# Optimization experiments

Measured on AMD Instinct MI355X. Metric: run time of the kernel, lower is better.

Reference implementation:

```python
import jax, jax.numpy as jnp
import numpy as np

# Grid / problem constants (match init_kwargs: shape=[15,400,400], batch_size=2)
B, D, H, W = 2, 15, 400, 400
N = 200000          # active voxels
CIN, COUT = 32, 64
# 27 kernel offsets for ksize=3, dilation=1, centered (submanifold alignment)
OFFS = np.array([[dz, dy, dx]
                 for dz in (-1, 0, 1)
                 for dy in (-1, 0, 1)
                 for dx in (-1, 0, 1)], dtype=np.int32)  # [27, 3]


def setup_inputs() -> dict:
    rng = np.random.default_rng(0)
    # unique active voxel coordinates (sorted flat indices for locality)
    flat = np.sort(rng.choice(B * D * H * W, size=N, replace=False)).astype(np.int64)
    b = flat // (D * H * W)
    r = flat % (D * H * W)
    z = r // (H * W)
    r = r % (H * W)
    y = r // W
    x = r % W
    coors = jnp.asarray(np.stack([b, z, y, x], axis=1).astype(np.int32))  # [N,4]

    key = jax.random.key(0)
    k1, k2, k3 = jax.random.split(key, 3)
    features = jax.random.normal(k1, (N, CIN), jnp.float32)
    W1 = jax.random.normal(k2, (27, CIN, COUT), jnp.float32) * (1.0 / np.sqrt(27.0 * CIN))
    W2 = jax.random.normal(k3, (27, COUT, COUT), jnp.float32) * (1.0 / np.sqrt(27.0 * COUT))
    return {"features": features, "coors": coors, "batch_size": B, "W1": W1, "W2": W2}


def _neighbor_table(coors):
    """Rulebook: for each of 27 offsets, index of the neighboring active voxel (-1 if none)."""
    n = coors.shape[0]
    flat = ((coors[:, 0] * D + coors[:, 1]) * H + coors[:, 2]) * W + coors[:, 3]
    # dense voxel hash: flat coord -> row index, -1 = inactive
    table = jnp.full((B * D * H * W,), -1, jnp.int32).at[flat].set(
        jnp.arange(n, dtype=jnp.int32))
    offs = jnp.asarray(OFFS)  # [27,3]
    z = coors[None, :, 1] + offs[:, 0:1]  # [27,N]
    y = coors[None, :, 2] + offs[:, 1:2]
    x = coors[None, :, 3] + offs[:, 2:3]
    valid = (z >= 0) & (z < D) & (y >= 0) & (y < H) & (x >= 0) & (x < W)
    nflat = ((coors[None, :, 0] * D + jnp.clip(z, 0, D - 1)) * H
             + jnp.clip(y, 0, H - 1)) * W + jnp.clip(x, 0, W - 1)
    nbr = table[nflat]                      # [27, N]
    return jnp.where(valid, nbr, -1)


def _subm_conv(feats, nbr, Wk):
    """Gather-GEMM-scatter submanifold conv: out[i] = sum_k W[k] @ feats[nbr[k,i]]."""
    out = jnp.zeros((feats.shape[0], Wk.shape[-1]), feats.dtype)
    for k in range(nbr.shape[0]):  # fixed 27-iteration loop over kernel offsets
        j = nbr[k]
        valid = j >= 0
        g = jnp.where(valid[:, None], feats[jnp.where(valid, j, 0)], 0.0)  # [N,Cin]
        out = out + g @ Wk[k]
    return out


def reference(features, coors, batch_size, W1, W2):
    # Submanifold conv preserves the active set -> rulebook is shared by both layers.
    nbr = _neighbor_table(coors)
    x = _subm_conv(features, nbr, W1)   # [N, COUT]
    x = _subm_conv(x, nbr, W2)          # [N, COUT]
    return x
```

## Files before the change

kernel.cpp:

```cpp
#include <hip/hip_runtime.h>
#include <hip/hip_bf16.h>

#define DD 15
#define HH 400
#define WW 400
#define CIN 32
#define COUT 64
#define KK 27
#define NVOX (2 * DD * HH * WW)
#define NWORDS (NVOX / 64)
#define CAP 32768
#define CNT_STRIDE 64
#define OFFC_GRID 2048
#define PCAP 262144
#define SCAN_B 1024

typedef short bf16x8 __attribute__((ext_vector_type(8)));
typedef float f32x4  __attribute__((ext_vector_type(4)));

__device__ inline short f2bf(float f) {
    unsigned u = __float_as_uint(f);
    return (short)((u + 0x7FFFu + ((u >> 16) & 1u)) >> 16);
}
__device__ inline float bflo(unsigned u) { return __uint_as_float(u << 16); }
__device__ inline float bfhi(unsigned u) { return __uint_as_float(u & 0xFFFF0000u); }

__global__ void init_kernel(unsigned long long* __restrict__ bitmap,
                            int* __restrict__ cnt) {
    int t = blockIdx.x * blockDim.x + threadIdx.x;
    if (t < KK * CNT_STRIDE) cnt[t] = 0;
    int stride = gridDim.x * blockDim.x;
    for (int w = t; w < NWORDS; w += stride) bitmap[w] = 0ull;
}

__global__ void fill_kernel(const int* __restrict__ coors,
                            int* __restrict__ flats,
                            unsigned long long* __restrict__ bitmap, int n) {
    int i = blockIdx.x * blockDim.x + threadIdx.x;
    if (i >= n) return;
    int b = coors[i * 4 + 0];
    int z = coors[i * 4 + 1];
    int y = coors[i * 4 + 2];
    int x = coors[i * 4 + 3];
    int f = ((b * DD + z) * HH + y) * WW + x;
    flats[i] = f;
    atomicOr(&bitmap[f >> 6], 1ull << (f & 63));
}

__global__ void prefix_kernel(const int* __restrict__ flats,
                              int* __restrict__ prefix, int n) {
    int w = blockIdx.x * blockDim.x + threadIdx.x;
    if (w >= NWORDS) return;
    int target = w << 6;
    int lo = 0, hi = n;
    while (lo < hi) {
        int mid = (lo + hi) >> 1;
        if (flats[mid] < target) lo = mid + 1; else hi = mid;
    }
    prefix[w] = lo;
}

__device__ inline bool bm_test(const unsigned long long* __restrict__ bitmap, int f) {
    return (bitmap[f >> 6] >> (f & 63)) & 1ull;
}
__device__ inline int bm_rank(const unsigned long long* __restrict__ bitmap,
                              const int* __restrict__ prefix, int f) {
    int w = f >> 6, b = f & 63;
    unsigned long long m = bitmap[w];
    return prefix[w] + __popcll(m & ((1ull << b) - 1ull));
}

__global__ __launch_bounds__(256) void build_pairs_kernel(
        const int* __restrict__ flats,
        const unsigned long long* __restrict__ bitmap,
        const int* __restrict__ prefix,
        int* __restrict__ cnt, int* __restrict__ pairI,
        int* __restrict__ pairJ, int* __restrict__ percnt, int n) {
    __shared__ int lcnt[KK];
    __shared__ int lbase[KK];
    __shared__ int lpos[KK];
    int i = blockIdx.x * blockDim.x + threadIdx.x;
    if (threadIdx.x < KK) { lcnt[threadIdx.x] = 0; lpos[threadIdx.x] = 0; }
    __syncthreads();

    int f0 = 0, x = 0;
    unsigned vmask = 0;
    bool act = (i < n);
    if (act) {
        f0 = flats[i];
        x = f0 % WW;
        int rem = f0 / WW;
        int y = rem % HH;
        int z = (rem / HH) % DD;
#pragma unroll
        for (int p = 0; p < 9; ++p) {
            int dz = p / 3 - 1, dy = p % 3 - 1;
            int zn = z + dz, yn = y + dy;
            if (zn < 0 || zn >= DD || yn < 0 || yn >= HH) continue;
            int fn = f0 + dz * (HH * WW) + dy * WW;
            int kb = p * 3;
            if (x > 0 && bm_test(bitmap, fn - 1)) {
                vmask |= 1u << kb; atomicAdd(&lcnt[kb], 1);
            }
            if (kb + 1 != 13 && bm_test(bitmap, fn)) {
                vmask |= 1u << (kb + 1); atomicAdd(&lcnt[kb + 1], 1);
            }
            if (x < WW - 1 && bm_test(bitmap, fn + 1)) {
                vmask |= 1u << (kb + 2); atomicAdd(&lcnt[kb + 2], 1);
            }
        }
        percnt[i] = __popc(vmask);
    }
    __syncthreads();
    if (threadIdx.x < KK && lcnt[threadIdx.x] > 0)
        lbase[threadIdx.x] = atomicAdd(&cnt[threadIdx.x * CNT_STRIDE], lcnt[threadIdx.x]);
    __syncthreads();
    if (act && vmask) {
        int lt = 0;
#pragma unroll
        for (int p = 0; p < 9; ++p) {
            int kb = p * 3;
            if (!(vmask & (7u << kb))) continue;
            int dz = p / 3 - 1, dy = p % 3 - 1;
            int fn = f0 + dz * (HH * WW) + dy * WW;
#pragma unroll
            for (int d = 0; d < 3; ++d) {
                int k = kb + d;
                if (!(vmask & (1u << k))) continue;
                int j = bm_rank(bitmap, prefix, fn + d - 1);
                int pos = lbase[k] + atomicAdd(&lpos[k], 1);
                if (pos < CAP) {
                    pairI[k * CAP + pos] = (i << 5) | lt;
                    pairJ[k * CAP + pos] = j;
                }
                ++lt;
            }
        }
    }
}

__global__ void pad_pairs_kernel(const int* __restrict__ cnt,
                                 int* __restrict__ pairI,
                                 int* __restrict__ pairJ, int n) {
    int k = blockIdx.x;
    int ck = min(cnt[k * CNT_STRIDE], CAP);
    int ckp = min((ck + 127) & ~127, CAP);
    for (int pos = ck + (int)threadIdx.x; pos < ckp; pos += blockDim.x) {
        pairI[k * CAP + pos] = (n << 5);
        pairJ[k * CAP + pos] = 0;
    }
}

__global__ void scan1_kernel(const int* __restrict__ pc, int* __restrict__ bsum, int n) {
    __shared__ int red[256];
    int base = blockIdx.x * SCAN_B;
    int s = 0;
#pragma unroll
    for (int u = 0; u < 4; ++u) {
        int idx = base + u * 256 + threadIdx.x;
        if (idx < n) s += pc[idx];
    }
    red[threadIdx.x] = s; __syncthreads();
    for (int o = 128; o > 0; o >>= 1) {
        if ((int)threadIdx.x < o) red[threadIdx.x] += red[threadIdx.x + o];
        __syncthreads();
    }
    if (threadIdx.x == 0) bsum[blockIdx.x] = red[0];
}

__global__ void scan2_kernel(int* __restrict__ bsum, int nb) {
    __shared__ int s[256];
    int v = ((int)threadIdx.x < nb) ? bsum[threadIdx.x] : 0;
    s[threadIdx.x] = v; __syncthreads();
    for (int o = 1; o < 256; o <<= 1) {
        int t = ((int)threadIdx.x >= o) ? s[threadIdx.x - o] : 0;
        __syncthreads();
        s[threadIdx.x] += t;
        __syncthreads();
    }
    if ((int)threadIdx.x < nb) bsum[threadIdx.x] = s[threadIdx.x] - v;
}

__global__ void scan3_kernel(const int* __restrict__ pc, const int* __restrict__ bsum,
                             int* __restrict__ rowptr, int n) {
    __shared__ int ts[256];
    int base = blockIdx.x * SCAN_B + threadIdx.x * 4;
    int e[4]; int s = 0;
#pragma unroll
    for (int u = 0; u < 4; ++u) {
        int idx = base + u;
        e[u] = (idx < n) ? pc[idx] : 0;
        s += e[u];
    }
    ts[threadIdx.x] = s; __syncthreads();
    for (int o = 1; o < 256; o <<= 1) {
        int t = ((int)threadIdx.x >= o) ? ts[threadIdx.x - o] : 0;
        __syncthreads();
        ts[threadIdx.x] += t;
        __syncthreads();
    }
    int run = ts[threadIdx.x] - s + bsum[blockIdx.x];
#pragma unroll
    for (int u = 0; u < 4; ++u) {
        int idx = base + u;
        if (idx < n) rowptr[idx] = run;
        run += e[u];
        if (idx == n - 1) rowptr[n] = run;
    }
}

template <int C>
__global__ __launch_bounds__(256) void center_mfma_kernel(
        const float* __restrict__ xin, const float* __restrict__ Wc,
        const int* __restrict__ rowptr, const unsigned short* __restrict__ part,
        float* __restrict__ xout, int n) {
    constexpr int KT = C / 32;
    int lane = threadIdx.x & 63;
    int mrow = lane & 15;
    int kgrp = lane >> 4;
    int wid = (blockIdx.x * blockDim.x + threadIdx.x) >> 6;
    int nwaves = (gridDim.x * blockDim.x) >> 6;

    bf16x8 bf[KT][4];
#pragma unroll
    for (int kt = 0; kt < KT; ++kt)
#pragma unroll
        for (int nt = 0; nt < 4; ++nt)
#pragma unroll
            for (int j = 0; j < 8; ++j)
                bf[kt][nt][j] = f2bf(Wc[(kt * 32 + kgrp * 8 + j) * 64 + nt * 16 + mrow]);

    int ntiles = (n + 15) >> 4;
    for (int t = wid; t < ntiles; t += nwaves) {
        int row = t * 16 + mrow;
        f32x4 zero = {0.f, 0.f, 0.f, 0.f};
        bf16x8 a[KT];
        if (row < n) {
            const float* xr = xin + (size_t)row * C + kgrp * 8;
#pragma unroll
            for (int kt = 0; kt < KT; ++kt) {
                float4 x0 = *(const float4*)(xr + kt * 32);
                float4 x1 = *(const float4*)(xr + kt * 32 + 4);
                a[kt][0] = f2bf(x0.x); a[kt][1] = f2bf(x0.y);
                a[kt][2] = f2bf(x0.z); a[kt][3] = f2bf(x0.w);
                a[kt][4] = f2bf(x1.x); a[kt][5] = f2bf(x1.y);
                a[kt][6] = f2bf(x1.z); a[kt][7] = f2bf(x1.w);
            }
        } else {
#pragma unroll
            for (int kt = 0; kt < KT; ++kt)
#pragma unroll
                for (int j = 0; j < 8; ++j) a[kt][j] = 0;
        }
        f32x4 acc[4];
#pragma unroll
        for (int nt = 0; nt < 4; ++nt) {
            acc[nt] = zero;
#pragma unroll
            for (int kt = 0; kt < KT; ++kt)
                acc[nt] = __builtin_amdgcn_mfma_f32_16x16x32_bf16(a[kt], bf[kt][nt], acc[nt], 0, 0, 0);
        }
#pragma unroll
        for (int r = 0; r < 4; ++r) {
            int orow = t * 16 + kgrp * 4 + r;
            if (orow < n) {
                int s0 = rowptr[orow], s1 = rowptr[orow + 1];
                for (int s = s0; s < s1; ++s) {
                    uint2 q = *(const uint2*)(part + (size_t)s * 64 + mrow * 4);
                    acc[0][r] += bflo(q.x);
                    acc[1][r] += bfhi(q.x);
                    acc[2][r] += bflo(q.y);
                    acc[3][r] += bfhi(q.y);
                }
#pragma unroll
                for (int nt = 0; nt < 4; ++nt)
                    xout[(size_t)orow * 64 + nt * 16 + mrow] = acc[nt][r];
            }
        }
    }
}

template <int C>
__global__ __launch_bounds__(256) void offc_mfma_kernel(
        const float* __restrict__ xin, const float* __restrict__ Wsrc,
        const int* __restrict__ cnt, const int* __restrict__ pairI,
        const int* __restrict__ pairJ, const int* __restrict__ rowptr,
        unsigned short* __restrict__ part, int n) {
    constexpr int KT = C / 32;
    __shared__ int pfx[KK + 1];
    int lane = threadIdx.x & 63;
    int wid = threadIdx.x >> 6;
    int mrow = lane & 15;
    int kgrp = lane >> 4;
    if (threadIdx.x == 0) {
        int acc = 0; pfx[0] = 0;
        for (int k = 0; k < KK; ++k) {
            int ck = min(cnt[k * CNT_STRIDE], CAP);
            acc += (ck + 127) >> 7;
            pfx[k + 1] = acc;
        }
    }
    __syncthreads();
    int T = pfx[KK];
    for (int g = blockIdx.x; g < T; g += gridDim.x) {
        int k = 0;
        while (pfx[k + 1] <= g) ++k;
        int chunk = g - pfx[k];
        const float* Wk = Wsrc + (size_t)k * C * 64;
        bf16x8 bf[KT][4];
#pragma unroll
        for (int kt = 0; kt < KT; ++kt)
#pragma unroll
            for (int nt = 0; nt < 4; ++nt)
#pragma unroll
                for (int j = 0; j < 8; ++j)
                    bf[kt][nt][j] = f2bf(Wk[(kt * 32 + kgrp * 8 + j) * 64 + nt * 16 + mrow]);
        int base = k * CAP + chunk * 128 + wid * 32;
#pragma unroll
        for (int half = 0; half < 2; ++half) {
            int b16 = base + half * 16;
            int jrow = pairJ[b16 + mrow];
            const float* xr = xin + (size_t)jrow * C + kgrp * 8;
            bf16x8 a[KT];
#pragma unroll
            for (int kt = 0; kt < KT; ++kt) {
                float4 x0 = *(const float4*)(xr + kt * 32);
                float4 x1 = *(const float4*)(xr + kt * 32 + 4);
                a[kt][0] = f2bf(x0.x); a[kt][1] = f2bf(x0.y);
                a[kt][2] = f2bf(x0.z); a[kt][3] = f2bf(x0.w);
                a[kt][4] = f2bf(x1.x); a[kt][5] = f2bf(x1.y);
                a[kt][6] = f2bf(x1.z); a[kt][7] = f2bf(x1.w);
            }
            f32x4 zero = {0.f, 0.f, 0.f, 0.f};
            f32x4 acc[4];
#pragma unroll
            for (int nt = 0; nt < 4; ++nt) {
                acc[nt] = zero;
#pragma unroll
                for (int kt = 0; kt < KT; ++kt)
                    acc[nt] = __builtin_amdgcn_mfma_f32_16x16x32_bf16(a[kt], bf[kt][nt], acc[nt], 0, 0, 0);
            }
#pragma unroll
            for (int r = 0; r < 4; ++r) {
                int pk = pairI[b16 + kgrp * 4 + r];
                int ir = pk >> 5;
                if (ir < n) {
                    int dst = rowptr[ir] + (pk & 31);
                    if (dst < PCAP) {
                        uint2 q;
                        q.x = (unsigned)(unsigned short)f2bf(acc[0][r]) |
                              ((unsigned)(unsigned short)f2bf(acc[1][r]) << 16);
                        q.y = (unsigned)(unsigned short)f2bf(acc[2][r]) |
                              ((unsigned)(unsigned short)f2bf(acc[3][r]) << 16);
                        *(uint2*)(part + (size_t)dst * 64 + mrow * 4) = q;
                    }
                }
            }
        }
    }
}

extern "C" void kernel_launch(void* const* d_in, const int* in_sizes, int n_in,
                              void* d_out, int out_size, void* d_ws, size_t ws_size,
                              hipStream_t stream) {
    const float* feats = (const float*)d_in[0];
    const int*   coors = (const int*)d_in[1];
    const float* W1 = (const float*)d_in[3];
    const float* W2 = (const float*)d_in[4];
    float* out = (float*)d_out;

    int n = in_sizes[0] / CIN;

    char* ws = (char*)d_ws;
    size_t off = 0;
    float* x1 = (float*)(ws + off);
    off += ((size_t)n * COUT * 4 + 255) & ~(size_t)255;
    unsigned long long* bitmap = (unsigned long long*)(ws + off);
    off += ((size_t)NWORDS * 8 + 255) & ~(size_t)255;
    int* prefix = (int*)(ws + off);
    off += ((size_t)NWORDS * 4 + 255) & ~(size_t)255;
    int* flats = (int*)(ws + off);
    off += ((size_t)n * 4 + 255) & ~(size_t)255;
    int* percnt = (int*)(ws + off);
    off += ((size_t)n * 4 + 255) & ~(size_t)255;
    int* rowptr = (int*)(ws + off);
    off += ((size_t)(n + 1) * 4 + 255) & ~(size_t)255;
    int* bsum = (int*)(ws + off);
    off += (256 * 4 + 255) & ~(size_t)255;
    int* cnt = (int*)(ws + off);
    off += ((size_t)KK * CNT_STRIDE * 4 + 255) & ~(size_t)255;
    int* pairI = (int*)(ws + off);
    off += ((size_t)KK * CAP * 4 + 4096 + 255) & ~(size_t)255;
    int* pairJ = (int*)(ws + off);
    off += ((size_t)KK * CAP * 4 + 4096 + 255) & ~(size_t)255;
    unsigned short* part = (unsigned short*)(ws + off);

    int nscan = (n + SCAN_B - 1) / SCAN_B;
    int ntiles = (n + 15) / 16;
    int cgrid = (ntiles + 3) / 4;

    init_kernel<<<(NWORDS + 255) / 256, 256, 0, stream>>>(bitmap, cnt);
    fill_kernel<<<(n + 255) / 256, 256, 0, stream>>>(coors, flats, bitmap, n);
    prefix_kernel<<<(NWORDS + 255) / 256, 256, 0, stream>>>(flats, prefix, n);
    build_pairs_kernel<<<(n + 255) / 256, 256, 0, stream>>>(
        flats, bitmap, prefix, cnt, pairI, pairJ, percnt, n);
    pad_pairs_kernel<<<KK, 256, 0, stream>>>(cnt, pairI, pairJ, n);
    scan1_kernel<<<nscan, 256, 0, stream>>>(percnt, bsum, n);
    scan2_kernel<<<1, 256, 0, stream>>>(bsum, nscan);
    scan3_kernel<<<nscan, 256, 0, stream>>>(percnt, bsum, rowptr, n);
    offc_mfma_kernel<CIN><<<OFFC_GRID, 256, 0, stream>>>(
        feats, W1, cnt, pairI, pairJ, rowptr, part, n);
    center_mfma_kernel<CIN><<<cgrid, 256, 0, stream>>>(
        feats, W1 + (size_t)13 * CIN * COUT, rowptr, part, x1, n);
    offc_mfma_kernel<COUT><<<OFFC_GRID, 256, 0, stream>>>(
        x1, W2, cnt, pairI, pairJ, rowptr, part, n);
    center_mfma_kernel<COUT><<<cgrid, 256, 0, stream>>>(
        x1, W2 + (size_t)13 * COUT * COUT, rowptr, part, out, n);
}
```

Before: 160.0 us.

## Store intermediate activations in bf16 and fold scan and padding kernels together

The first-layer output x1 is now written as bf16 instead of fp32. The second layer's gather and center kernels then load bf16x8 vectors directly, with no float-to-bf16 conversion. The pad-pairs kernel is merged into the first scan pass as extra blocks, and the single-block scan2 is removed by having each scan3 block reduce the preceding block sums itself. Together these halve intermediate traffic and cut two kernel launches. The cost is a redundant block-sum reduction in every scan3 block; precision is unchanged because the MFMA inputs were already rounded to bf16.

```diff
diff --git a/kernel.cpp b/kernel.cpp
--- a/kernel.cpp
+++ b/kernel.cpp
@@ -139,20 +139,20 @@
     }
 }
 
-__global__ void pad_pairs_kernel(const int* __restrict__ cnt,
-                                 int* __restrict__ pairI,
-                                 int* __restrict__ pairJ, int n) {
-    int k = blockIdx.x;
-    int ck = min(cnt[k * CNT_STRIDE], CAP);
-    int ckp = min((ck + 127) & ~127, CAP);
-    for (int pos = ck + (int)threadIdx.x; pos < ckp; pos += blockDim.x) {
-        pairI[k * CAP + pos] = (n << 5);
-        pairJ[k * CAP + pos] = 0;
-    }
-}
-
-__global__ void scan1_kernel(const int* __restrict__ pc, int* __restrict__ bsum, int n) {
+__global__ void scan1pad_kernel(const int* __restrict__ pc, int* __restrict__ bsum,
+                                const int* __restrict__ cnt, int* __restrict__ pairI,
+                                int* __restrict__ pairJ, int n, int nscan) {
     __shared__ int red[256];
+    if ((int)blockIdx.x >= nscan) {
+        int k = blockIdx.x - nscan;
+        int ck = min(cnt[k * CNT_STRIDE], CAP);
+        int ckp = min((ck + 127) & ~127, CAP);
+        for (int pos = ck + (int)threadIdx.x; pos < ckp; pos += blockDim.x) {
+            pairI[k * CAP + pos] = (n << 5);
+            pairJ[k * CAP + pos] = 0;
+        }
+        return;
+    }
     int base = blockIdx.x * SCAN_B;
     int s = 0;
 #pragma unroll
@@ -168,22 +168,19 @@
     if (threadIdx.x == 0) bsum[blockIdx.x] = red[0];
 }
 
-__global__ void scan2_kernel(int* __restrict__ bsum, int nb) {
-    __shared__ int s[256];
-    int v = ((int)threadIdx.x < nb) ? bsum[threadIdx.x] : 0;
-    s[threadIdx.x] = v; __syncthreads();
-    for (int o = 1; o < 256; o <<= 1) {
-        int t = ((int)threadIdx.x >= o) ? s[threadIdx.x - o] : 0;
+__global__ void scan3_kernel(const int* __restrict__ pc, const int* __restrict__ bsum,
+                             int* __restrict__ rowptr, int n, int nscan) {
+    __shared__ int ts[256];
+    __shared__ int bs[256];
+    int v = ((int)threadIdx.x < nscan && (int)threadIdx.x < (int)blockIdx.x)
+                ? bsum[threadIdx.x] : 0;
+    bs[threadIdx.x] = v; __syncthreads();
+    for (int o = 128; o > 0; o >>= 1) {
+        if ((int)threadIdx.x < o) bs[threadIdx.x] += bs[threadIdx.x + o];
         __syncthreads();
-        s[threadIdx.x] += t;
-        __syncthreads();
-    }
-    if ((int)threadIdx.x < nb) bsum[threadIdx.x] = s[threadIdx.x] - v;
-}
-
-__global__ void scan3_kernel(const int* __restrict__ pc, const int* __restrict__ bsum,
-                             int* __restrict__ rowptr, int n) {
-    __shared__ int ts[256];
+    }
+    int bbase = bs[0];
+
     int base = blockIdx.x * SCAN_B + threadIdx.x * 4;
     int e[4]; int s = 0;
 #pragma unroll
@@ -199,7 +196,7 @@
         ts[threadIdx.x] += t;
         __syncthreads();
     }
-    int run = ts[threadIdx.x] - s + bsum[blockIdx.x];
+    int run = ts[threadIdx.x] - s + bbase;
 #pragma unroll
     for (int u = 0; u < 4; ++u) {
         int idx = base + u;
@@ -209,11 +206,11 @@
     }
 }
 
-template <int C>
+template <int C, typename TIN, typename TOUT>
 __global__ __launch_bounds__(256) void center_mfma_kernel(
-        const float* __restrict__ xin, const float* __restrict__ Wc,
+        const TIN* __restrict__ xin, const float* __restrict__ Wc,
         const int* __restrict__ rowptr, const unsigned short* __restrict__ part,
-        float* __restrict__ xout, int n) {
+        TOUT* __restrict__ xout, int n) {
     constexpr int KT = C / 32;
     int lane = threadIdx.x & 63;
     int mrow = lane & 15;
@@ -236,15 +233,22 @@
         f32x4 zero = {0.f, 0.f, 0.f, 0.f};
         bf16x8 a[KT];
         if (row < n) {
-            const float* xr = xin + (size_t)row * C + kgrp * 8;
-#pragma unroll
-            for (int kt = 0; kt < KT; ++kt) {
-                float4 x0 = *(const float4*)(xr + kt * 32);
-                float4 x1 = *(const float4*)(xr + kt * 32 + 4);
-                a[kt][0] = f2bf(x0.x); a[kt][1] = f2bf(x0.y);
-                a[kt][2] = f2bf(x0.z); a[kt][3] = f2bf(x0.w);
-                a[kt][4] = f2bf(x1.x); a[kt][5] = f2bf(x1.y);
-                a[kt][6] = f2bf(x1.z); a[kt][7] = f2bf(x1.w);
+            if constexpr (sizeof(TIN) == 4) {
+                const float* xr = (const float*)xin + (size_t)row * C + kgrp * 8;
+#pragma unroll
+                for (int kt = 0; kt < KT; ++kt) {
+                    float4 x0 = *(const float4*)(xr + kt * 32);
+                    float4 x1 = *(const float4*)(xr + kt * 32 + 4);
+                    a[kt][0] = f2bf(x0.x); a[kt][1] = f2bf(x0.y);
+                    a[kt][2] = f2bf(x0.z); a[kt][3] = f2bf(x0.w);
+                    a[kt][4] = f2bf(x1.x); a[kt][5] = f2bf(x1.y);
+                    a[kt][6] = f2bf(x1.z); a[kt][7] = f2bf(x1.w);
+                }
+            } else {
+                const unsigned short* xr = (const unsigned short*)xin + (size_t)row * C + kgrp * 8;
+#pragma unroll
+                for (int kt = 0; kt < KT; ++kt)
+                    a[kt] = *(const bf16x8*)(xr + kt * 32);
             }
         } else {
 #pragma unroll
@@ -272,17 +276,24 @@
                     acc[2][r] += bflo(q.y);
                     acc[3][r] += bfhi(q.y);
                 }
-#pragma unroll
-                for (int nt = 0; nt < 4; ++nt)
-                    xout[(size_t)orow * 64 + nt * 16 + mrow] = acc[nt][r];
-            }
-        }
-    }
-}
-
-template <int C>
+                if constexpr (sizeof(TOUT) == 4) {
+#pragma unroll
+                    for (int nt = 0; nt < 4; ++nt)
+                        ((float*)xout)[(size_t)orow * 64 + nt * 16 + mrow] = acc[nt][r];
+                } else {
+#pragma unroll
+                    for (int nt = 0; nt < 4; ++nt)
+                        ((unsigned short*)xout)[(size_t)orow * 64 + nt * 16 + mrow] =
+                            (unsigned short)f2bf(acc[nt][r]);
+                }
+            }
+        }
+    }
+}
+
+template <int C, typename TIN>
 __global__ __launch_bounds__(256) void offc_mfma_kernel(
-        const float* __restrict__ xin, const float* __restrict__ Wsrc,
+        const TIN* __restrict__ xin, const float* __restrict__ Wsrc,
         const int* __restrict__ cnt, const int* __restrict__ pairI,
         const int* __restrict__ pairJ, const int* __restrict__ rowptr,
         unsigned short* __restrict__ part, int n) {
@@ -320,16 +331,23 @@
         for (int half = 0; half < 2; ++half) {
             int b16 = base + half * 16;
             int jrow = pairJ[b16 + mrow];
-            const float* xr = xin + (size_t)jrow * C + kgrp * 8;
             bf16x8 a[KT];
-#pragma unroll
-            for (int kt = 0; kt < KT; ++kt) {
-                float4 x0 = *(const float4*)(xr + kt * 32);
-                float4 x1 = *(const float4*)(xr + kt * 32 + 4);
-                a[kt][0] = f2bf(x0.x); a[kt][1] = f2bf(x0.y);
-                a[kt][2] = f2bf(x0.z); a[kt][3] = f2bf(x0.w);
-                a[kt][4] = f2bf(x1.x); a[kt][5] = f2bf(x1.y);
-                a[kt][6] = f2bf(x1.z); a[kt][7] = f2bf(x1.w);
+            if constexpr (sizeof(TIN) == 4) {
+                const float* xr = (const float*)xin + (size_t)jrow * C + kgrp * 8;
+#pragma unroll
+                for (int kt = 0; kt < KT; ++kt) {
+                    float4 x0 = *(const float4*)(xr + kt * 32);
+                    float4 x1 = *(const float4*)(xr + kt * 32 + 4);
+                    a[kt][0] = f2bf(x0.x); a[kt][1] = f2bf(x0.y);
+                    a[kt][2] = f2bf(x0.z); a[kt][3] = f2bf(x0.w);
+                    a[kt][4] = f2bf(x1.x); a[kt][5] = f2bf(x1.y);
+                    a[kt][6] = f2bf(x1.z); a[kt][7] = f2bf(x1.w);
+                }
+            } else {
+                const unsigned short* xr = (const unsigned short*)xin + (size_t)jrow * C + kgrp * 8;
+#pragma unroll
+                for (int kt = 0; kt < KT; ++kt)
+                    a[kt] = *(const bf16x8*)(xr + kt * 32);
             }
             f32x4 zero = {0.f, 0.f, 0.f, 0.f};
             f32x4 acc[4];
@@ -373,8 +391,8 @@
 
     char* ws = (char*)d_ws;
     size_t off = 0;
-    float* x1 = (float*)(ws + off);
-    off += ((size_t)n * COUT * 4 + 255) & ~(size_t)255;
+    unsigned short* x1 = (unsigned short*)(ws + off);
+    off += ((size_t)n * COUT * 2 + 255) & ~(size_t)255;
     unsigned long long* bitmap = (unsigned long long*)(ws + off);
     off += ((size_t)NWORDS * 8 + 255) & ~(size_t)255;
     int* prefix = (int*)(ws + off);
@@ -404,16 +422,14 @@
     prefix_kernel<<<(NWORDS + 255) / 256, 256, 0, stream>>>(flats, prefix, n);
     build_pairs_kernel<<<(n + 255) / 256, 256, 0, stream>>>(
         flats, bitmap, prefix, cnt, pairI, pairJ, percnt, n);
-    pad_pairs_kernel<<<KK, 256, 0, stream>>>(cnt, pairI, pairJ, n);
-    scan1_kernel<<<nscan, 256, 0, stream>>>(percnt, bsum, n);
-    scan2_kernel<<<1, 256, 0, stream>>>(bsum, nscan);
-    scan3_kernel<<<nscan, 256, 0, stream>>>(percnt, bsum, rowptr, n);
-    offc_mfma_kernel<CIN><<<OFFC_GRID, 256, 0, stream>>>(
+    scan1pad_kernel<<<nscan + KK, 256, 0, stream>>>(percnt, bsum, cnt, pairI, pairJ, n, nscan);
+    scan3_kernel<<<nscan, 256, 0, stream>>>(percnt, bsum, rowptr, n, nscan);
+    offc_mfma_kernel<CIN, float><<<OFFC_GRID, 256, 0, stream>>>(
         feats, W1, cnt, pairI, pairJ, rowptr, part, n);
-    center_mfma_kernel<CIN><<<cgrid, 256, 0, stream>>>(
+    center_mfma_kernel<CIN, float, unsigned short><<<cgrid, 256, 0, stream>>>(
         feats, W1 + (size_t)13 * CIN * COUT, rowptr, part, x1, n);
-    offc_mfma_kernel<COUT><<<OFFC_GRID, 256, 0, stream>>>(
+    offc_mfma_kernel<COUT, unsigned short><<<OFFC_GRID, 256, 0, stream>>>(
         x1, W2, cnt, pairI, pairJ, rowptr, part, n);
-    center_mfma_kernel<COUT><<<cgrid, 256, 0, stream>>>(
+    center_mfma_kernel<COUT, unsigned short, float><<<cgrid, 256, 0, stream>>>(
         x1, W2 + (size_t)13 * COUT * COUT, rowptr, part, out, n);
 }
```

Measured after the change: 150.6 us. 5.9% less time.
